# Optimization experiments

Measured on AMD Instinct MI355X. Metric: run time of the kernel, lower is better.

Reference implementation:

```python
import jax, jax.numpy as jnp
import numpy as np

D_MODEL = 1024
N_HEAD = 16
HEAD_DIM = D_MODEL // N_HEAD
N_POS = 4096
K_PROJ = 256  # self.k is hardcoded to 256 in the module
BATCH = 4


def setup_inputs() -> dict:
    key = jax.random.key(0)
    ks = jax.random.split(key, 11)
    s = 1.0 / np.sqrt(D_MODEL)
    return {
        "x": jax.random.normal(ks[0], (BATCH, N_POS, D_MODEL), jnp.float32),
        "Wq": jax.random.normal(ks[1], (D_MODEL, D_MODEL), jnp.float32) * s,
        "bq": jnp.zeros((D_MODEL,), jnp.float32),
        "Wk": jax.random.normal(ks[2], (D_MODEL, D_MODEL), jnp.float32) * s,
        "bk": jnp.zeros((D_MODEL,), jnp.float32),
        "Wv": jax.random.normal(ks[3], (D_MODEL, D_MODEL), jnp.float32) * s,
        "bv": jnp.zeros((D_MODEL,), jnp.float32),
        "E": jax.random.normal(ks[4], (K_PROJ, N_POS), jnp.float32),
        "F": jax.random.normal(ks[5], (K_PROJ, N_POS), jnp.float32),
        "Wo": jax.random.normal(ks[6], (D_MODEL, D_MODEL), jnp.float32) * s,
        "bo": jnp.zeros((D_MODEL,), jnp.float32),
    }


def reference(x, Wq, bq, Wk, bk, Wv, bv, E, F, Wo, bo):
    B, N, D = x.shape
    scale = jnp.sqrt(jnp.asarray(HEAD_DIM, x.dtype))
    # Q/K/V projections (nn.Linear applies x @ W.T + b)
    def proj(W, b):
        y = jnp.einsum('bnd,ed->bne', x, W) + b
        return y.reshape(B, N, N_HEAD, HEAD_DIM).transpose(0, 2, 1, 3)  # bhnd
    Q = proj(Wq, bq)
    K = proj(Wk, bk)
    V = proj(Wv, bv)
    # Linformer low-rank projections along sequence dim
    Kp = jnp.einsum('kn,bhnd->bhkd', E, K)
    Vp = jnp.einsum('kn,bhnd->bhkd', F, V)
    attn_score = jnp.einsum('bhnd,bhkd->bhnk', Q, Kp) / scale
    attn = jax.nn.softmax(attn_score, axis=-1)  # dropout is identity (drop_prob=0)
    out = jnp.einsum('bhnk,bhkd->bhnd', attn, Vp)
    out = out.transpose(0, 2, 1, 3).reshape(B, N, D)
    out = jnp.einsum('bnd,ed->bne', out, Wo) + bo
    return out, attn_score
```

## Files before the change

### kernel.cpp

```cpp
#include <hip/hip_runtime.h>

typedef _Float16 f16;
typedef __attribute__((ext_vector_type(8))) _Float16 f16x8;
typedef __attribute__((ext_vector_type(4))) _Float16 f16x4;
typedef __attribute__((ext_vector_type(4))) float f32x4;

typedef const __attribute__((address_space(1))) unsigned int* gas_ptr;
typedef __attribute__((address_space(3))) unsigned int* las_ptr;

__device__ __forceinline__ void gload16(const f16* g, f16* l) {
  __builtin_amdgcn_global_load_lds((gas_ptr)g, (las_ptr)l, 16, 0, 0);
}

template<int WM, int WN, bool OUT32>
__device__ __forceinline__ void gemm_core(
    const f16* __restrict__ A, int lda,
    const f16* __restrict__ B, int ldb,
    int kLen,
    f16* lsA, f16* lsB,
    float* __restrict__ C32, f16* __restrict__ C16, int ldc,
    float scale, const float* __restrict__ biasC, const float* __restrict__ biasR)
{
  constexpr int T   = WM * WN * 64;
  constexpr int nA  = (WM * 64 * 8) / T;
  constexpr int nB  = (WN * 64 * 8) / T;
  constexpr int RPI = T / 8;
  const int t    = threadIdx.x;
  const int lane = t & 63;
  const int wave = t >> 6;
  const int wm   = wave / WN;
  const int wn   = wave % WN;

  f32x4 acc[4][4];
  const f32x4 z4 = {0.f, 0.f, 0.f, 0.f};
#pragma unroll
  for (int i = 0; i < 4; ++i)
#pragma unroll
    for (int j = 0; j < 4; ++j) acc[i][j] = z4;

  const int r_ = t >> 3;
  const int c_ = (t & 7) * 8;
  const int ldsOff = (wave << 9);

  for (int kt = 0; kt < kLen; kt += 64) {
#pragma unroll
    for (int i = 0; i < nA; ++i) {
      const f16* g = A + (size_t)(i * RPI + r_) * lda + kt + c_;
      gload16(g, lsA + i * (T * 8) + ldsOff);
    }
#pragma unroll
    for (int i = 0; i < nB; ++i) {
      const f16* g = B + (size_t)(i * RPI + r_) * ldb + kt + c_;
      gload16(g, lsB + i * (T * 8) + ldsOff);
    }
    __syncthreads();
#pragma unroll
    for (int ks = 0; ks < 2; ++ks) {
      f16x8 af[4], bf[4];
#pragma unroll
      for (int i = 0; i < 4; ++i)
        af[i] = *(const f16x8*)&lsA[(wm * 64 + i * 16 + (lane & 15)) * 64 + ks * 32 + (lane >> 4) * 8];
#pragma unroll
      for (int j = 0; j < 4; ++j)
        bf[j] = *(const f16x8*)&lsB[(wn * 64 + j * 16 + (lane & 15)) * 64 + ks * 32 + (lane >> 4) * 8];
#pragma unroll
      for (int i = 0; i < 4; ++i)
#pragma unroll
        for (int j = 0; j < 4; ++j)
          acc[i][j] = __builtin_amdgcn_mfma_f32_16x16x32_f16(af[i], bf[j], acc[i][j], 0, 0, 0);
    }
    __syncthreads();
  }

  const int lc = lane & 15;
  const int lr = (lane >> 4) * 4;
#pragma unroll
  for (int j = 0; j < 4; ++j) {
    const int col = wn * 64 + j * 16 + lc;
    const float bC = biasC ? biasC[col] : 0.f;
#pragma unroll
    for (int i = 0; i < 4; ++i) {
      const int rbase = wm * 64 + i * 16 + lr;
#pragma unroll
      for (int r = 0; r < 4; ++r) {
        const int row = rbase + r;
        float v = acc[i][j][r] * scale + bC;
        if (biasR) v += biasR[row];
        if (OUT32) C32[(size_t)row * ldc + col] = v;
        else       C16[(size_t)row * ldc + col] = (f16)v;
      }
    }
  }
}

template<bool OUT32>
__global__ __launch_bounds__(512) void k_gemm256(
    const f16* __restrict__ A, int lda,
    const f16* __restrict__ B, int ldb,
    int kLen, int nct,
    float* __restrict__ C32, f16* __restrict__ C16, int ldc,
    const float* __restrict__ biasC)
{
  __shared__ f16 ls[4][2][8192];

  const int cpx = gridDim.x >> 3;
  const int wg  = (blockIdx.x & 7) * cpx + (blockIdx.x >> 3);
  const int rt  = wg / nct, ct = wg % nct;

  const int t    = threadIdx.x;
  const int lane = t & 63;
  const int w    = t >> 6;
  const int wm   = w >> 2;
  const int wn   = w & 3;
  const int c    = lane & 15;
  const int g    = lane >> 4;
  const int ch   = c >> 1;
  const int c1   = c & 1;
  const int jsw  = (g ^ (ch & 3)) << 4;

  const f16* Ab = A + (size_t)rt * 256 * lda;
  const f16* Bb = B + (size_t)ct * 256 * ldb;

  const int srow = ((t >> 3) << 1) + ((t >> 2) & 1);
  const int sj   = ((t & 3) ^ ((t >> 3) & 3)) * 8;
  const int NT   = kLen >> 5;

#define STAGE_A(tile) { const int kt_ = (tile) * 32; f16* d_ = &ls[(tile) & 3][0][0]; \
    gload16(Ab + (size_t)srow * lda + kt_ + sj, d_ + t * 8); \
    gload16(Ab + (size_t)(srow + 128) * lda + kt_ + sj, d_ + 4096 + t * 8); }
#define STAGE_B(tile) { const int kt_ = (tile) * 32; f16* d_ = &ls[(tile) & 3][1][0]; \
    gload16(Bb + (size_t)srow * ldb + kt_ + sj, d_ + t * 8); \
    gload16(Bb + (size_t)(srow + 128) * ldb + kt_ + sj, d_ + 4096 + t * 8); }

  STAGE_A(0); STAGE_B(0);
  STAGE_A(1); STAGE_B(1);
  asm volatile("s_waitcnt vmcnt(4)" ::: "memory");
  __builtin_amdgcn_s_barrier();

  f32x4 acc[8][4];
  const f32x4 z4 = {0.f, 0.f, 0.f, 0.f};
#pragma unroll
  for (int i = 0; i < 8; ++i)
#pragma unroll
    for (int j = 0; j < 4; ++j) acc[i][j] = z4;

  for (int tt = 0; tt < NT; ++tt) {
    const char* lA = (const char*)&ls[tt & 3][0][0];
    const char* lB = (const char*)&ls[tt & 3][1][0];
    f16x8 af[8], bf[4];
#pragma unroll
    for (int mf = 0; mf < 4; ++mf)
      af[mf] = *(const f16x8*)(lA + (size_t)(wm * 64 + mf * 8 + ch) * 128 + c1 * 64 + jsw);
#pragma unroll
    for (int nf = 0; nf < 4; ++nf)
      bf[nf] = *(const f16x8*)(lB + (size_t)(wn * 32 + nf * 8 + ch) * 128 + c1 * 64 + jsw);
    if (tt + 2 < NT) STAGE_A(tt + 2);
    __builtin_amdgcn_s_barrier();
    __builtin_amdgcn_s_setprio(1);
#pragma unroll
    for (int mf = 0; mf < 4; ++mf)
#pragma unroll
      for (int nf = 0; nf < 4; ++nf)
        acc[mf][nf] = __builtin_amdgcn_mfma_f32_16x16x32_f16(af[mf], bf[nf], acc[mf][nf], 0, 0, 0);
    __builtin_amdgcn_s_setprio(0);
#pragma unroll
    for (int mf = 4; mf < 8; ++mf)
      af[mf] = *(const f16x8*)(lA + (size_t)(wm * 64 + mf * 8 + ch) * 128 + c1 * 64 + jsw);
    if (tt + 2 < NT) {
      STAGE_B(tt + 2);
      asm volatile("s_waitcnt vmcnt(4)" ::: "memory");
    } else {
      asm volatile("s_waitcnt vmcnt(0)" ::: "memory");
    }
    __builtin_amdgcn_s_barrier();
    __builtin_amdgcn_s_setprio(1);
#pragma unroll
    for (int mf = 4; mf < 8; ++mf)
#pragma unroll
      for (int nf = 0; nf < 4; ++nf)
        acc[mf][nf] = __builtin_amdgcn_mfma_f32_16x16x32_f16(af[mf], bf[nf], acc[mf][nf], 0, 0, 0);
    __builtin_amdgcn_s_setprio(0);
  }
#undef STAGE_A
#undef STAGE_B

#pragma unroll
  for (int nf = 0; nf < 4; ++nf) {
    const int col = ct * 256 + wn * 64 + nf * 16 + c;
    const float bC = biasC ? biasC[col] : 0.f;
#pragma unroll
    for (int mf = 0; mf < 8; ++mf) {
      const int rbase = rt * 256 + wm * 128 + mf * 16 + g * 4;
#pragma unroll
      for (int r = 0; r < 4; ++r) {
        const float v = acc[mf][nf][r] + bC;
        if (OUT32) __builtin_nontemporal_store(v, C32 + (size_t)(rbase + r) * ldc + col);
        else       C16[(size_t)(rbase + r) * ldc + col] = (f16)v;
      }
    }
  }
}

template<int WM, int WN, bool OUT32>
__global__ __launch_bounds__(WM * WN * 64) void k_gemm(
    const f16* A, int lda, const f16* B, int ldb, int kLen,
    float* C32, f16* C16, int ldc, float scale,
    const float* biasC, const float* biasR)
{
  __shared__ f16 lsA[WM * 64 * 64];
  __shared__ f16 lsB[WN * 64 * 64];
  const size_t rt = blockIdx.y, ct = blockIdx.x;
  gemm_core<WM, WN, OUT32>(
      A + rt * (WM * 64) * (size_t)lda, lda,
      B + ct * (WN * 64) * (size_t)ldb, ldb, kLen,
      lsA, lsB,
      OUT32 ? C32 + rt * (WM * 64) * (size_t)ldc + ct * (WN * 64) : nullptr,
      OUT32 ? nullptr : C16 + rt * (WM * 64) * (size_t)ldc + ct * (WN * 64), ldc,
      scale,
      biasC ? biasC + ct * (WN * 64) : nullptr,
      biasR ? biasR + rt * (WM * 64) : nullptr);
}

__global__ __launch_bounds__(256) void k_cast_xt(const float* __restrict__ x,
                                                 f16* __restrict__ Xf,
                                                 f16* __restrict__ XT)
{
  __shared__ f16 tile[64][68];
  const int b = blockIdx.z, bi = blockIdx.y, bj = blockIdx.x;
  const int r0 = threadIdx.x >> 4;
  const int c4 = (threadIdx.x & 15) * 4;
  const float* xb = x + ((size_t)b * 4096 + (size_t)bi * 64) * 1024 + bj * 64;
#pragma unroll
  for (int rr = 0; rr < 4; ++rr) {
    const int row = rr * 16 + r0;
    const float4 v = *(const float4*)(xb + (size_t)row * 1024 + c4);
    f16x4 h = {(f16)v.x, (f16)v.y, (f16)v.z, (f16)v.w};
    *(f16x4*)&tile[row][c4] = h;
    *(f16x4*)(Xf + ((size_t)b * 4096 + (size_t)bi * 64 + row) * 1024 + bj * 64 + c4) = h;
  }
  __syncthreads();
#pragma unroll
  for (int rr = 0; rr < 4; ++rr) {
    const int col = rr * 16 + r0;
    f16x4 h = {tile[c4 + 0][col], tile[c4 + 1][col], tile[c4 + 2][col], tile[c4 + 3][col]};
    *(f16x4*)(XT + ((size_t)b * 1024 + (size_t)bj * 64 + col) * 4096 + (size_t)bi * 64 + c4) = h;
  }
}

__global__ __launch_bounds__(256) void k_cast_w(
    const float* w0, const float* w1, const float* w2,
    const float* w3, const float* w4, const float* w5, f16* __restrict__ d)
{
  const size_t i = ((size_t)blockIdx.x * 256 + threadIdx.x) * 4;
  const int seg = (int)(i >> 20);
  const float* s = (seg == 0) ? w0 : (seg == 1) ? w1 : (seg == 2) ? w2
                 : (seg == 3) ? w3 : (seg == 4) ? w4 : w5;
  const float4 v = *(const float4*)(s + (i & 1048575));
  f16x4 o = {(f16)v.x, (f16)v.y, (f16)v.z, (f16)v.w};
  *(f16x4*)(d + i) = o;
}

__global__ __launch_bounds__(256) void k_rowsum(const float* __restrict__ E,
                                                const float* __restrict__ F,
                                                float* __restrict__ rs)
{
  const int r = blockIdx.x * 4 + (threadIdx.x >> 6);
  const int lane = threadIdx.x & 63;
  const float* src = (r < 256) ? (E + (size_t)r * 4096) : (F + (size_t)(r - 256) * 4096);
  float s = 0.f;
#pragma unroll
  for (int i = 0; i < 16; ++i) {
    const float4 v = *(const float4*)(src + i * 256 + lane * 4);
    s += v.x + v.y + v.z + v.w;
  }
#pragma unroll
  for (int o = 32; o; o >>= 1) s += __shfl_xor(s, o);
  if (lane == 0) rs[r] = s;
}

__global__ __launch_bounds__(256) void k_exfx(const f16* __restrict__ EF,
                                              const f16* __restrict__ XT,
                                              float* __restrict__ part)
{
  __shared__ f16 lsA[128 * 64];
  __shared__ f16 lsB[128 * 64];
  const int z = blockIdx.z; const int b = z & 3; const int s = z >> 2;
  const int rt = blockIdx.y, ct = blockIdx.x;
  const f16* A = EF + (size_t)rt * 128 * 4096 + s * 1024;
  const f16* B = XT + (size_t)b * 1024 * 4096 + (size_t)ct * 128 * 4096 + s * 1024;
  float* C = part + (size_t)z * (512 * 1024) + (size_t)rt * 128 * 1024 + ct * 128;
  gemm_core<2, 2, true>(A, 4096, B, 4096, 1024, lsA, lsB, C, nullptr, 1024, 1.f, nullptr, nullptr);
}

__global__ __launch_bounds__(256) void k_reduce2(const float* __restrict__ part,
                                                 f16* __restrict__ EXf)
{
  const size_t i = ((size_t)blockIdx.x * 256 + threadIdx.x) * 4;
  const size_t b = i >> 19;
  const size_t idx = i & 524287;
  const float4 a = *(const float4*)(part + (0 * 4 + b) * 524288 + idx);
  const float4 c1 = *(const float4*)(part + (1 * 4 + b) * 524288 + idx);
  const float4 c2 = *(const float4*)(part + (2 * 4 + b) * 524288 + idx);
  const float4 c3 = *(const float4*)(part + (3 * 4 + b) * 524288 + idx);
  f16x4 o = {(f16)(a.x + c1.x + c2.x + c3.x), (f16)(a.y + c1.y + c2.y + c3.y),
             (f16)(a.z + c1.z + c2.z + c3.z), (f16)(a.w + c1.w + c2.w + c3.w)};
  *(f16x4*)(EXf + i) = o;
}

__global__ __launch_bounds__(256) void k_kpvp(const f16* __restrict__ EXf,
                                              const f16* __restrict__ W16,
                                              float* __restrict__ p2)
{
  __shared__ f16 lsA[128 * 64];
  __shared__ f16 lsB[128 * 64];
  const int z = blockIdx.z; const int which = z & 1; const int s = z >> 1;
  const int rt = blockIdx.y, ct = blockIdx.x;
  const f16 *A, *B;
  if (which == 0) {
    const int b = rt >> 1, r0 = (rt & 1) * 128;
    A = EXf + ((size_t)b * 512 + r0) * 1024 + s * 512;
    B = W16 + 1048576 + (size_t)ct * 128 * 1024 + s * 512;
  } else {
    const int b = ct >> 1, r0 = (ct & 1) * 128;
    A = W16 + 2 * 1048576 + (size_t)rt * 128 * 1024 + s * 512;
    B = EXf + ((size_t)b * 512 + 256 + r0) * 1024 + s * 512;
  }
  float* C = p2 + (size_t)(s * 2 + which) * 1048576 + (size_t)rt * 128 * 1024 + ct * 128;
  gemm_core<2, 2, true>(A, 1024, B, 1024, 512, lsA, lsB, C, nullptr, 1024, 1.f, nullptr, nullptr);
}

__global__ __launch_bounds__(256) void k_reduce3(const float* __restrict__ p2,
                                                 f16* __restrict__ KpVp,
                                                 const float* __restrict__ rs,
                                                 const float* __restrict__ bk,
                                                 const float* __restrict__ bv)
{
  const size_t i = ((size_t)blockIdx.x * 256 + threadIdx.x) * 4;
  const int half = (int)(i >> 20);
  const size_t j = i & 1048575;
  size_t pidx; float r1[4];
  if (half == 0) {
    const int r  = (int)((j >> 10) & 255);
    const int hd = (int)(j & 1023);
    pidx = j;
    const float se = rs[r];
#pragma unroll
    for (int t = 0; t < 4; ++t) r1[t] = se * bk[hd + t];
  } else {
    const int b  = (int)(j >> 18);
    const int hd = (int)((j >> 8) & 1023);
    const int r  = (int)(j & 255);
    pidx = (size_t)hd * 1024 + (size_t)b * 256 + r;
    const float bb = bv[hd];
#pragma unroll
    for (int t = 0; t < 4; ++t) r1[t] = bb * rs[256 + r + t];
  }
  const float4 a = *(const float4*)(p2 + (size_t)(0 * 2 + half) * 1048576 + pidx);
  const float4 c = *(const float4*)(p2 + (size_t)(1 * 2 + half) * 1048576 + pidx);
  f16x4 o = {(f16)(a.x + c.x + r1[0]), (f16)(a.y + c.y + r1[1]),
             (f16)(a.z + c.z + r1[2]), (f16)(a.w + c.w + r1[3])};
  *(f16x4*)(KpVp + i) = o;
}

__global__ __launch_bounds__(256) void k_attn(const f16* __restrict__ Q,
                                              const f16* __restrict__ Kp,
                                              const f16* __restrict__ VpT,
                                              float* __restrict__ S,
                                              f16* __restrict__ OP)
{
  __shared__ char smem[98304];
  f16* lsK = (f16*)smem;
  f16* lsQ = (f16*)(smem + 32768);
  f16* lsV = (f16*)(smem + 65536);

  const int rt = blockIdx.x, h = blockIdx.y, b = blockIdx.z;
  const int t = threadIdx.x, lane = t & 63, w = t >> 6;
  const int g = lane >> 4;
  const int c = lane & 15;

  const int r_ = t >> 3;
  const int cswz = ((t & 7) * 16) ^ ((r_ & 7) << 4);
  const char* Kg = (const char*)(Kp + (size_t)b * 262144 + h * 64);
  const char* Qg = (const char*)(Q + ((size_t)b * 4096 + (size_t)rt * 128) * 1024 + h * 64);
#pragma unroll
  for (int i = 0; i < 8; ++i)
    gload16((const f16*)(Kg + (size_t)(i * 32 + r_) * 2048 + cswz),
            lsK + i * 2048 + (w << 9));
#pragma unroll
  for (int i = 0; i < 4; ++i)
    gload16((const f16*)(Qg + (size_t)(i * 32 + r_) * 2048 + cswz),
            lsQ + i * 2048 + (w << 9));
  {
    const char* Vb = (const char*)(VpT + ((size_t)b * 1024 + h * 64) * 256);
    const int vrow = lane >> 5;
    const int voff = (lane & 31) * 16;
#pragma unroll
    for (int i = 0; i < 8; ++i) {
      const int row = i * 8 + w * 2 + vrow;
      const int so = voff ^ ((row & 7) << 4);
      gload16((const f16*)(Vb + (size_t)row * 512 + so),
              (f16*)((char*)lsV + i * 4096 + w * 1024));
    }
  }
  __syncthreads();

  const int swz = (lane & 7) << 4;
  f32x4 acc[16][2];
  const f32x4 z4 = {0.f, 0.f, 0.f, 0.f};
#pragma unroll
  for (int i = 0; i < 16; ++i) { acc[i][0] = z4; acc[i][1] = z4; }
#pragma unroll
  for (int ks = 0; ks < 2; ++ks) {
    const int koff = ks * 64 + g * 16;
    f16x8 bf[2];
#pragma unroll
    for (int j = 0; j < 2; ++j) {
      const int row = w * 32 + j * 16 + c;
      bf[j] = *(const f16x8*)((const char*)lsQ + row * 128 + (koff ^ swz));
    }
#pragma unroll
    for (int i = 0; i < 16; ++i) {
      const f16x8 af = *(const f16x8*)((const char*)lsK + (i * 16 + c) * 128 + (koff ^ swz));
      acc[i][0] = __builtin_amdgcn_mfma_f32_16x16x32_f16(af, bf[0], acc[i][0], 0, 0, 0);
      acc[i][1] = __builtin_amdgcn_mfma_f32_16x16x32_f16(af, bf[1], acc[i][1], 0, 0, 0);
    }
  }

  float* Sb = S + (((size_t)(b * 16 + h)) * 4096 + (size_t)rt * 128 + w * 32) * 256;
#pragma unroll
  for (int j = 0; j < 2; ++j)
#pragma unroll
    for (int i = 0; i < 16; ++i) {
      acc[i][j] *= 0.125f;
      __builtin_nontemporal_store(acc[i][j],
          (f32x4*)(Sb + (size_t)(j * 16 + c) * 256 + i * 16 + g * 4));
    }

  float pinv[2];
#pragma unroll
  for (int j = 0; j < 2; ++j) {
    float m = acc[0][j][0];
#pragma unroll
    for (int i = 0; i < 16; ++i)
      m = fmaxf(m, fmaxf(fmaxf(acc[i][j][0], acc[i][j][1]),
                         fmaxf(acc[i][j][2], acc[i][j][3])));
    m = fmaxf(m, __shfl_xor(m, 16));
    m = fmaxf(m, __shfl_xor(m, 32));
    float s = 0.f;
#pragma unroll
    for (int i = 0; i < 16; ++i)
#pragma unroll
      for (int r2 = 0; r2 < 4; ++r2) {
        const float e = __expf(acc[i][j][r2] - m);
        acc[i][j][r2] = e;
        s += e;
      }
    s += __shfl_xor(s, 16);
    s += __shfl_xor(s, 32);
    pinv[j] = 1.f / s;
  }

  __syncthreads();
  char* lsP = (char*)smem;
#pragma unroll
  for (int j = 0; j < 2; ++j) {
    const int n = w * 32 + j * 16 + c;
    char* base = lsP + n * 512;
#pragma unroll
    for (int i = 0; i < 16; ++i) {
      f16x4 p = {(f16)(acc[i][j][0] * pinv[j]), (f16)(acc[i][j][1] * pinv[j]),
                 (f16)(acc[i][j][2] * pinv[j]), (f16)(acc[i][j][3] * pinv[j])};
      *(f16x4*)(base + ((i * 32 + g * 8) ^ swz)) = p;
    }
  }
  __syncthreads();

  f32x4 o[2][4];
#pragma unroll
  for (int i2 = 0; i2 < 2; ++i2)
#pragma unroll
    for (int jh = 0; jh < 4; ++jh) o[i2][jh] = z4;
#pragma unroll
  for (int ks = 0; ks < 8; ++ks) {
    const int koff = ks * 64 + g * 16;
    f16x8 pa[2];
#pragma unroll
    for (int i2 = 0; i2 < 2; ++i2) {
      const int n = w * 32 + i2 * 16 + c;
      pa[i2] = *(const f16x8*)(lsP + n * 512 + (koff ^ swz));
    }
#pragma unroll
    for (int jh = 0; jh < 4; ++jh) {
      const f16x8 vb = *(const f16x8*)((const char*)lsV + (jh * 16 + c) * 512 + (koff ^ swz));
      o[0][jh] = __builtin_amdgcn_mfma_f32_16x16x32_f16(pa[0], vb, o[0][jh], 0, 0, 0);
      o[1][jh] = __builtin_amdgcn_mfma_f32_16x16x32_f16(pa[1], vb, o[1][jh], 0, 0, 0);
    }
  }

  f16* Ob = OP + ((size_t)b * 4096 + (size_t)rt * 128 + w * 32) * 1024 + h * 64;
#pragma unroll
  for (int jh = 0; jh < 4; ++jh) {
    const int col = jh * 16 + c;
#pragma unroll
    for (int i2 = 0; i2 < 2; ++i2) {
      const int rb = i2 * 16 + g * 4;
#pragma unroll
      for (int r2 = 0; r2 < 4; ++r2)
        Ob[(size_t)(rb + r2) * 1024 + col] = (f16)o[i2][jh][r2];
    }
  }
}

extern "C" void kernel_launch(void* const* d_in, const int* in_sizes, int n_in,
                              void* d_out, int out_size, void* d_ws, size_t ws_size,
                              hipStream_t stream) {
  const float* x  = (const float*)d_in[0];
  const float* Wq = (const float*)d_in[1];
  const float* bq = (const float*)d_in[2];
  const float* Wk = (const float*)d_in[3];
  const float* bk = (const float*)d_in[4];
  const float* Wv = (const float*)d_in[5];
  const float* bv = (const float*)d_in[6];
  const float* E  = (const float*)d_in[7];
  const float* F  = (const float*)d_in[8];
  const float* Wo = (const float*)d_in[9];
  const float* bo = (const float*)d_in[10];

  float* out = (float*)d_out;
  float* S   = out + 16777216;

  char* w = (char*)d_ws;
  f16*   Xf     = (f16*)w;
  f16*   EXf    = (f16*)w;
  float* rowsum = (float*)(w + 4 * 1048576);
  f16*   XT     = (f16*)(w + 33554432);
  f16*   OPf    = (f16*)(w + 33554432);
  f16*   Qf     = (f16*)(w + (size_t)2 * 33554432);
  float* part   = (float*)(w + (size_t)3 * 33554432);
  float* part2  = (float*)(w + (size_t)3 * 33554432);
  f16*   W16    = (f16*)(w + (size_t)4 * 33554432);
  f16*   EF16   = W16 + (size_t)4 * 1048576;
  f16*   KpVp   = (f16*)(w + (size_t)4 * 33554432 + 12582912);

  k_cast_xt<<<dim3(16, 64, 4), 256, 0, stream>>>(x, Xf, XT);
  k_cast_w<<<6144, 256, 0, stream>>>(Wq, Wk, Wv, Wo, E, F, W16);

  k_gemm256<false><<<256, 512, 0, stream>>>(
      Xf, 1024, W16, 1024, 1024, 4, nullptr, Qf, 1024, bq);

  k_rowsum<<<128, 256, 0, stream>>>(E, F, rowsum);

  k_exfx<<<dim3(8, 4, 16), 256, 0, stream>>>(EF16, XT, part);
  k_reduce2<<<2048, 256, 0, stream>>>(part, EXf);

  k_kpvp<<<dim3(8, 8, 4), 256, 0, stream>>>(EXf, W16, part2);
  k_reduce3<<<2048, 256, 0, stream>>>(part2, KpVp, rowsum, bk, bv);

  k_attn<<<dim3(32, 16, 4), 256, 0, stream>>>(
      Qf, KpVp, KpVp + (size_t)4 * 262144, S, OPf);

  k_gemm256<true><<<256, 512, 0, stream>>>(
      OPf, 1024, W16 + 3 * 1048576, 1024, 1024, 4, out, nullptr, 1024, bo);
}
```

Measured before the change: 599.5 us.

## Route E·X GEMM through 256-tile pipeline and shrink attention LDS for occupancy

Factors the 256x256 pipelined GEMM body into a reusable core and uses it for the E/F times X^T product, replacing the 128x128 gemm_core kernel. The split-K factor goes from 4 to 8 slices, and the reduction is updated to sum 8 partials, which are staged in the attention-score output buffer. Separately, the attention kernel keeps normalized probabilities in registers and writes them to LDS in two halves. This cuts LDS from 96KB to 80KB and adds launch_bounds(256,2) so two blocks can share a CU, at the cost of extra barriers and register pressure.

Result: no change. 606.6 us (+1.2%).

```diff
diff --git a/kernel.cpp b/kernel.cpp
--- a/kernel.cpp
+++ b/kernel.cpp
@@ -11,6 +11,11 @@
 __device__ __forceinline__ void gload16(const f16* g, f16* l) {
   __builtin_amdgcn_global_load_lds((gas_ptr)g, (las_ptr)l, 16, 0, 0);
 }
+
+#define BARRIER_LGKM() do { \
+    asm volatile("s_waitcnt lgkmcnt(0)" ::: "memory"); \
+    __builtin_amdgcn_sched_barrier(0); \
+    __builtin_amdgcn_s_barrier(); } while (0)
 
 template<int WM, int WN, bool OUT32>
 __device__ __forceinline__ void gemm_core(
@@ -94,19 +99,14 @@
 }
 
 template<bool OUT32>
-__global__ __launch_bounds__(512) void k_gemm256(
-    const f16* __restrict__ A, int lda,
-    const f16* __restrict__ B, int ldb,
-    int kLen, int nct,
+__device__ __forceinline__ void gemm256_core(
+    f16 (*ls)[2][8192],
+    const f16* __restrict__ Ab, int lda,
+    const f16* __restrict__ Bb, int ldb,
+    int kLen,
     float* __restrict__ C32, f16* __restrict__ C16, int ldc,
     const float* __restrict__ biasC)
 {
-  __shared__ f16 ls[4][2][8192];
-
-  const int cpx = gridDim.x >> 3;
-  const int wg  = (blockIdx.x & 7) * cpx + (blockIdx.x >> 3);
-  const int rt  = wg / nct, ct = wg % nct;
-
   const int t    = threadIdx.x;
   const int lane = t & 63;
   const int w    = t >> 6;
@@ -118,9 +118,6 @@
   const int c1   = c & 1;
   const int jsw  = (g ^ (ch & 3)) << 4;
 
-  const f16* Ab = A + (size_t)rt * 256 * lda;
-  const f16* Bb = B + (size_t)ct * 256 * ldb;
-
   const int srow = ((t >> 3) << 1) + ((t >> 2) & 1);
   const int sj   = ((t & 3) ^ ((t >> 3) & 3)) * 8;
   const int NT   = kLen >> 5;
@@ -186,11 +183,11 @@
 
 #pragma unroll
   for (int nf = 0; nf < 4; ++nf) {
-    const int col = ct * 256 + wn * 64 + nf * 16 + c;
+    const int col = wn * 64 + nf * 16 + c;
     const float bC = biasC ? biasC[col] : 0.f;
 #pragma unroll
     for (int mf = 0; mf < 8; ++mf) {
-      const int rbase = rt * 256 + wm * 128 + mf * 16 + g * 4;
+      const int rbase = wm * 128 + mf * 16 + g * 4;
 #pragma unroll
       for (int r = 0; r < 4; ++r) {
         const float v = acc[mf][nf][r] + bC;
@@ -201,24 +198,44 @@
   }
 }
 
-template<int WM, int WN, bool OUT32>
-__global__ __launch_bounds__(WM * WN * 64) void k_gemm(
-    const f16* A, int lda, const f16* B, int ldb, int kLen,
-    float* C32, f16* C16, int ldc, float scale,
-    const float* biasC, const float* biasR)
-{
-  __shared__ f16 lsA[WM * 64 * 64];
-  __shared__ f16 lsB[WN * 64 * 64];
-  const size_t rt = blockIdx.y, ct = blockIdx.x;
-  gemm_core<WM, WN, OUT32>(
-      A + rt * (WM * 64) * (size_t)lda, lda,
-      B + ct * (WN * 64) * (size_t)ldb, ldb, kLen,
-      lsA, lsB,
-      OUT32 ? C32 + rt * (WM * 64) * (size_t)ldc + ct * (WN * 64) : nullptr,
-      OUT32 ? nullptr : C16 + rt * (WM * 64) * (size_t)ldc + ct * (WN * 64), ldc,
-      scale,
-      biasC ? biasC + ct * (WN * 64) : nullptr,
-      biasR ? biasR + rt * (WM * 64) : nullptr);
+template<bool OUT32>
+__global__ __launch_bounds__(512) void k_gemm256(
+    const f16* __restrict__ A, int lda,
+    const f16* __restrict__ B, int ldb,
+    int kLen, int nct,
+    float* __restrict__ C32, f16* __restrict__ C16, int ldc,
+    const float* __restrict__ biasC)
+{
+  __shared__ f16 ls[4][2][8192];
+  const int cpx = gridDim.x >> 3;
+  const int wg  = (blockIdx.x & 7) * cpx + (blockIdx.x >> 3);
+  const int rt  = wg / nct, ct = wg % nct;
+  gemm256_core<OUT32>(ls,
+      A + (size_t)rt * 256 * lda, lda,
+      B + (size_t)ct * 256 * ldb, ldb, kLen,
+      OUT32 ? C32 + (size_t)rt * 256 * ldc + ct * 256 : nullptr,
+      OUT32 ? nullptr : C16 + (size_t)rt * 256 * ldc + ct * 256, ldc,
+      biasC ? biasC + ct * 256 : nullptr);
+}
+
+__global__ __launch_bounds__(512) void k_exfx256(const f16* __restrict__ EF,
+                                                 const f16* __restrict__ XT,
+                                                 float* __restrict__ part)
+{
+  __shared__ f16 ls[4][2][8192];
+  const int cpx = gridDim.x >> 3;
+  const int wg  = (blockIdx.x & 7) * cpx + (blockIdx.x >> 3);
+  const int s   = wg >> 5;
+  const int rem = wg & 31;
+  const int b   = rem >> 3;
+  const int tile = rem & 7;
+  const int rt  = tile >> 2, ct = tile & 3;
+  gemm256_core<true>(ls,
+      EF + (size_t)rt * 256 * 4096 + s * 512, 4096,
+      XT + (size_t)b * 1024 * 4096 + (size_t)ct * 256 * 4096 + s * 512, 4096,
+      512,
+      part + (size_t)(s * 4 + b) * 524288 + (size_t)rt * 256 * 1024 + ct * 256,
+      nullptr, 1024, nullptr);
 }
 
 __global__ __launch_bounds__(256) void k_cast_xt(const float* __restrict__ x,
@@ -278,32 +295,19 @@
   if (lane == 0) rs[r] = s;
 }
 
-__global__ __launch_bounds__(256) void k_exfx(const f16* __restrict__ EF,
-                                              const f16* __restrict__ XT,
-                                              float* __restrict__ part)
-{
-  __shared__ f16 lsA[128 * 64];
-  __shared__ f16 lsB[128 * 64];
-  const int z = blockIdx.z; const int b = z & 3; const int s = z >> 2;
-  const int rt = blockIdx.y, ct = blockIdx.x;
-  const f16* A = EF + (size_t)rt * 128 * 4096 + s * 1024;
-  const f16* B = XT + (size_t)b * 1024 * 4096 + (size_t)ct * 128 * 4096 + s * 1024;
-  float* C = part + (size_t)z * (512 * 1024) + (size_t)rt * 128 * 1024 + ct * 128;
-  gemm_core<2, 2, true>(A, 4096, B, 4096, 1024, lsA, lsB, C, nullptr, 1024, 1.f, nullptr, nullptr);
-}
-
 __global__ __launch_bounds__(256) void k_reduce2(const float* __restrict__ part,
                                                  f16* __restrict__ EXf)
 {
   const size_t i = ((size_t)blockIdx.x * 256 + threadIdx.x) * 4;
   const size_t b = i >> 19;
   const size_t idx = i & 524287;
-  const float4 a = *(const float4*)(part + (0 * 4 + b) * 524288 + idx);
-  const float4 c1 = *(const float4*)(part + (1 * 4 + b) * 524288 + idx);
-  const float4 c2 = *(const float4*)(part + (2 * 4 + b) * 524288 + idx);
-  const float4 c3 = *(const float4*)(part + (3 * 4 + b) * 524288 + idx);
-  f16x4 o = {(f16)(a.x + c1.x + c2.x + c3.x), (f16)(a.y + c1.y + c2.y + c3.y),
-             (f16)(a.z + c1.z + c2.z + c3.z), (f16)(a.w + c1.w + c2.w + c3.w)};
+  float a0 = 0.f, a1 = 0.f, a2 = 0.f, a3 = 0.f;
+#pragma unroll
+  for (int s = 0; s < 8; ++s) {
+    const float4 v = *(const float4*)(part + ((size_t)s * 4 + b) * 524288 + idx);
+    a0 += v.x; a1 += v.y; a2 += v.z; a3 += v.w;
+  }
+  f16x4 o = {(f16)a0, (f16)a1, (f16)a2, (f16)a3};
   *(f16x4*)(EXf + i) = o;
 }
 
@@ -362,16 +366,16 @@
   *(f16x4*)(KpVp + i) = o;
 }
 
-__global__ __launch_bounds__(256) void k_attn(const f16* __restrict__ Q,
-                                              const f16* __restrict__ Kp,
-                                              const f16* __restrict__ VpT,
-                                              float* __restrict__ S,
-                                              f16* __restrict__ OP)
-{
-  __shared__ char smem[98304];
+__global__ __launch_bounds__(256, 2) void k_attn(const f16* __restrict__ Q,
+                                                 const f16* __restrict__ Kp,
+                                                 const f16* __restrict__ VpT,
+                                                 float* __restrict__ S,
+                                                 f16* __restrict__ OP)
+{
+  __shared__ char smem[81920];
   f16* lsK = (f16*)smem;
   f16* lsQ = (f16*)(smem + 32768);
-  f16* lsV = (f16*)(smem + 65536);
+  f16* lsV = (f16*)(smem + 49152);
 
   const int rt = blockIdx.x, h = blockIdx.y, b = blockIdx.z;
   const int t = threadIdx.x, lane = t & 63, w = t >> 6;
@@ -436,7 +440,7 @@
           (f32x4*)(Sb + (size_t)(j * 16 + c) * 256 + i * 16 + g * 4));
     }
 
-  float pinv[2];
+  f16x4 pf[16][2];
 #pragma unroll
   for (int j = 0; j < 2; ++j) {
     float m = acc[0][j][0];
@@ -457,43 +461,50 @@
       }
     s += __shfl_xor(s, 16);
     s += __shfl_xor(s, 32);
-    pinv[j] = 1.f / s;
-  }
-
-  __syncthreads();
-  char* lsP = (char*)smem;
-#pragma unroll
-  for (int j = 0; j < 2; ++j) {
-    const int n = w * 32 + j * 16 + c;
-    char* base = lsP + n * 512;
+    const float inv = 1.f / s;
 #pragma unroll
     for (int i = 0; i < 16; ++i) {
-      f16x4 p = {(f16)(acc[i][j][0] * pinv[j]), (f16)(acc[i][j][1] * pinv[j]),
-                 (f16)(acc[i][j][2] * pinv[j]), (f16)(acc[i][j][3] * pinv[j])};
-      *(f16x4*)(base + ((i * 32 + g * 8) ^ swz)) = p;
-    }
-  }
-  __syncthreads();
-
+      f16x4 p = {(f16)(acc[i][j][0] * inv), (f16)(acc[i][j][1] * inv),
+                 (f16)(acc[i][j][2] * inv), (f16)(acc[i][j][3] * inv)};
+      pf[i][j] = p;
+    }
+  }
+
+  char* lsPh = (char*)smem;
   f32x4 o[2][4];
 #pragma unroll
   for (int i2 = 0; i2 < 2; ++i2)
 #pragma unroll
     for (int jh = 0; jh < 4; ++jh) o[i2][jh] = z4;
-#pragma unroll
-  for (int ks = 0; ks < 8; ++ks) {
-    const int koff = ks * 64 + g * 16;
-    f16x8 pa[2];
-#pragma unroll
-    for (int i2 = 0; i2 < 2; ++i2) {
-      const int n = w * 32 + i2 * 16 + c;
-      pa[i2] = *(const f16x8*)(lsP + n * 512 + (koff ^ swz));
-    }
-#pragma unroll
-    for (int jh = 0; jh < 4; ++jh) {
-      const f16x8 vb = *(const f16x8*)((const char*)lsV + (jh * 16 + c) * 512 + (koff ^ swz));
-      o[0][jh] = __builtin_amdgcn_mfma_f32_16x16x32_f16(pa[0], vb, o[0][jh], 0, 0, 0);
-      o[1][jh] = __builtin_amdgcn_mfma_f32_16x16x32_f16(pa[1], vb, o[1][jh], 0, 0, 0);
+
+#pragma unroll
+  for (int half = 0; half < 2; ++half) {
+    BARRIER_LGKM();
+#pragma unroll
+    for (int j = 0; j < 2; ++j) {
+      const int n = w * 32 + j * 16 + c;
+      char* base = lsPh + n * 256;
+#pragma unroll
+      for (int i8 = 0; i8 < 8; ++i8)
+        *(f16x4*)(base + ((i8 * 32 + g * 8) ^ swz)) = pf[half * 8 + i8][j];
+    }
+    BARRIER_LGKM();
+#pragma unroll
+    for (int ks4 = 0; ks4 < 4; ++ks4) {
+      const int koffP = ks4 * 64 + g * 16;
+      const int koffV = half * 256 + koffP;
+      f16x8 pa[2];
+#pragma unroll
+      for (int i2 = 0; i2 < 2; ++i2) {
+        const int n = w * 32 + i2 * 16 + c;
+        pa[i2] = *(const f16x8*)(lsPh + n * 256 + (koffP ^ swz));
+      }
+#pragma unroll
+      for (int jh = 0; jh < 4; ++jh) {
+        const f16x8 vb = *(const f16x8*)((const char*)lsV + (jh * 16 + c) * 512 + (koffV ^ swz));
+        o[0][jh] = __builtin_amdgcn_mfma_f32_16x16x32_f16(pa[0], vb, o[0][jh], 0, 0, 0);
+        o[1][jh] = __builtin_amdgcn_mfma_f32_16x16x32_f16(pa[1], vb, o[1][jh], 0, 0, 0);
+      }
     }
   }
 
@@ -536,11 +547,11 @@
   f16*   XT     = (f16*)(w + 33554432);
   f16*   OPf    = (f16*)(w + 33554432);
   f16*   Qf     = (f16*)(w + (size_t)2 * 33554432);
-  float* part   = (float*)(w + (size_t)3 * 33554432);
   float* part2  = (float*)(w + (size_t)3 * 33554432);
   f16*   W16    = (f16*)(w + (size_t)4 * 33554432);
   f16*   EF16   = W16 + (size_t)4 * 1048576;
   f16*   KpVp   = (f16*)(w + (size_t)4 * 33554432 + 12582912);
+  float* partEX = S;
 
   k_cast_xt<<<dim3(16, 64, 4), 256, 0, stream>>>(x, Xf, XT);
   k_cast_w<<<6144, 256, 0, stream>>>(Wq, Wk, Wv, Wo, E, F, W16);
@@ -550,8 +561,8 @@
 
   k_rowsum<<<128, 256, 0, stream>>>(E, F, rowsum);
 
-  k_exfx<<<dim3(8, 4, 16), 256, 0, stream>>>(EF16, XT, part);
-  k_reduce2<<<2048, 256, 0, stream>>>(part, EXf);
+  k_exfx256<<<256, 512, 0, stream>>>(EF16, XT, partEX);
+  k_reduce2<<<2048, 256, 0, stream>>>(partEX, EXf);
 
   k_kpvp<<<dim3(8, 8, 4), 256, 0, stream>>>(EXf, W16, part2);
   k_reduce3<<<2048, 256, 0, stream>>>(part2, KpVp, rowsum, bk, bv);
```
